# Performance work log

Hardware: AMD Instinct MI355X
Metric: run time of the kernel (lower is better)

The kernel has to match this reference:

```python
import jax, jax.numpy as jnp
import numpy as np

UNITS = 256

def _lstm_step(carry, idx, kernel, rec_kernel, bias, num_chars):
    h, c = carry
    x = jax.nn.one_hot(idx, num_chars, dtype=h.dtype)          # [B, num_chars]
    z = x @ kernel + h @ rec_kernel + bias                      # [B, 4*UNITS]
    i, f, g, o = jnp.split(z, 4, axis=-1)                       # Keras gate order i,f,c,o
    i = jax.nn.sigmoid(i)
    f = jax.nn.sigmoid(f)
    g = jnp.tanh(g)
    o = jax.nn.sigmoid(o)
    c_new = f * c + i * g
    h_new = o * jnp.tanh(c_new)
    return (h_new, c_new), None


def setup_inputs() -> dict:
    key = jax.random.key(0)
    ks = jax.random.split(key, 4)
    num_chars, batch, seq_len = 128, 1024, 512
    x = jax.random.randint(ks[0], (batch, seq_len), 0, num_chars, dtype=jnp.int32)
    kernel = jax.random.normal(ks[1], (num_chars, 4 * UNITS), dtype=jnp.float32) * 0.05
    rec_kernel = jax.random.normal(ks[2], (UNITS, 4 * UNITS), dtype=jnp.float32) * 0.05
    bias = jnp.zeros((4 * UNITS,), dtype=jnp.float32)
    dense_w = jax.random.normal(ks[3], (UNITS, num_chars), dtype=jnp.float32) * 0.05
    dense_b = jnp.zeros((num_chars,), dtype=jnp.float32)
    return {"x": x, "kernel": kernel, "rec_kernel": rec_kernel, "bias": bias,
            "dense_w": dense_w, "dense_b": dense_b}


def reference(x, kernel, rec_kernel, bias, dense_w, dense_b):
    batch = x.shape[0]
    num_chars = kernel.shape[0]
    h0 = jnp.zeros((batch, UNITS), dtype=kernel.dtype)
    c0 = jnp.zeros((batch, UNITS), dtype=kernel.dtype)
    step = lambda carry, idx: _lstm_step(carry, idx, kernel, rec_kernel, bias, num_chars)
    (h, _), _ = jax.lax.scan(step, (h0, c0), x.T)  # scan over time: [S, B]
    logits = h @ dense_w + dense_b                  # [B, num_chars]
    return jax.nn.softmax(logits, axis=-1)
```

## Files before the change

### kernel.cpp

```cpp
#include <hip/hip_runtime.h>
#include <cstdint>

typedef __bf16 bf16x8 __attribute__((ext_vector_type(8)));
typedef float  f32x4  __attribute__((ext_vector_type(4)));

union U4B { uint4 u; bf16x8 b; };
__device__ __forceinline__ bf16x8 as_bf(uint4 u) { U4B x; x.u = u; return x.b; }

__device__ __forceinline__ unsigned short f2b(float x) {
  unsigned int u = __float_as_uint(x);
  unsigned int r = (u + 0x7fffu + ((u >> 16) & 1u)) >> 16;
  return (unsigned short)r;
}
__device__ __forceinline__ float b2f(unsigned int bits_lo16) {
  return __uint_as_float(bits_lo16 << 16);
}

__device__ __forceinline__ float sigm(float x) {
  float e = __builtin_amdgcn_exp2f(x * -1.4426950408889634f);
  return __builtin_amdgcn_rcpf(1.0f + e);
}
__device__ __forceinline__ float tanh_fast(float x) {
  float e = __builtin_amdgcn_exp2f(x * 2.8853900817779268f);
  return 1.0f - 2.0f * __builtin_amdgcn_rcpf(e + 1.0f);
}

__global__ void prep_kernel(const float* __restrict__ rec,
                            const float* __restrict__ kern,
                            const float* __restrict__ bias,
                            const float* __restrict__ dw,
                            unsigned short* __restrict__ recT,
                            unsigned short* __restrict__ kb2,
                            unsigned short* __restrict__ dwT) {
  int id = blockIdx.x * 256 + threadIdx.x;
  if (id < 262144) {
    int colp = id >> 8, k = id & 255;
    int u = colp >> 2, g = colp & 3;
    recT[colp * 256 + k] = f2b(rec[k * 1024 + u + 256 * g]);
  } else if (id < 262144 + 131072) {
    int i = id - 262144;
    int ch = i >> 10, colp = i & 1023;
    int u = colp >> 2, g = colp & 3;
    int oc = u + 256 * g;
    kb2[ch * 1024 + colp] = f2b(kern[ch * 1024 + oc] + bias[oc]);
  } else {
    int i = id - 262144 - 131072;
    int cls = i >> 8, k = i & 255;
    dwT[cls * 256 + k] = f2b(dw[k * 128 + cls]);
  }
}

__global__ __launch_bounds__(512, 2) void lstm_kernel(
    const unsigned short* __restrict__ recT,
    const unsigned short* __restrict__ kb2,
    const unsigned short* __restrict__ dwT,
    const int* __restrict__ x,
    const float* __restrict__ dense_b,
    float* __restrict__ out) {
  __shared__ unsigned short h_buf[2][16][264];
  __shared__ int   x_lds[16][516];
  __shared__ float l_lds[16][132];

  const int tid   = threadIdx.x;
  const int lane  = tid & 63;
  const int wid   = tid >> 6;
  const int row16 = lane & 15;
  const int kg    = lane >> 4;
  const int rbase = blockIdx.x << 4;

  for (int e = tid; e < 16 * 512; e += 512) {
    int r = e >> 9, c = e & 511;
    x_lds[r][c] = x[(rbase + r) * 512 + c];
  }
  for (int e = tid; e < 16 * 264; e += 512) (&h_buf[0][0][0])[e] = 0;

  float c_state[8];
#pragma unroll
  for (int m = 0; m < 8; ++m) c_state[m] = 0.0f;

  const unsigned short* recBase = recT + ((wid * 128 + row16) * 256 + kg * 8);

  __syncthreads();

  for (int t = 0; t < 512; ++t) {
    const int cur = t & 1, nxt = cur ^ 1;

    int idx = x_lds[row16][t];
    const unsigned short* kbBase = kb2 + (idx * 1024 + wid * 128 + kg * 4);
    uint2 kq[8];
#pragma unroll
    for (int m = 0; m < 8; ++m) kq[m] = *(const uint2*)(kbBase + m * 16);

    uint4 hf[8];
#pragma unroll
    for (int k = 0; k < 8; ++k)
      hf[k] = *(const uint4*)&h_buf[cur][row16][k * 32 + kg * 8];

    f32x4 acc[8];
#pragma unroll
    for (int m = 0; m < 8; ++m) {
      uint4 af[8];
#pragma unroll
      for (int k = 0; k < 8; ++k)
        af[k] = *(const uint4*)(recBase + m * 4096 + k * 32);
      f32x4 a = {0.f, 0.f, 0.f, 0.f};
#pragma unroll
      for (int k = 0; k < 8; ++k)
        a = __builtin_amdgcn_mfma_f32_16x16x32_bf16(as_bf(af[k]), as_bf(hf[k]), a, 0, 0, 0);
      acc[m] = a;
    }

#pragma unroll
    for (int m = 0; m < 8; ++m) {
      float zi = acc[m][0] + b2f(kq[m].x & 0xffffu);
      float zf = acc[m][1] + b2f(kq[m].x >> 16);
      float zg = acc[m][2] + b2f(kq[m].y & 0xffffu);
      float zo = acc[m][3] + b2f(kq[m].y >> 16);
      float gi = sigm(zi);
      float gf = sigm(zf);
      float gg = tanh_fast(zg);
      float go = sigm(zo);
      float c  = gf * c_state[m] + gi * gg;
      c_state[m] = c;
      float h  = go * tanh_fast(c);
      h_buf[nxt][row16][(wid * 8 + m) * 4 + kg] = f2b(h);
    }
    __syncthreads();
  }

  {
    const unsigned short* dwBase = dwT + ((wid * 16 + row16) * 256 + kg * 8);
    uint4 hf[8];
#pragma unroll
    for (int k = 0; k < 8; ++k)
      hf[k] = *(const uint4*)&h_buf[0][row16][k * 32 + kg * 8];
    f32x4 la = {0.f, 0.f, 0.f, 0.f};
#pragma unroll
    for (int k = 0; k < 8; ++k) {
      uint4 af = *(const uint4*)(dwBase + k * 32);
      la = __builtin_amdgcn_mfma_f32_16x16x32_bf16(as_bf(af), as_bf(hf[k]), la, 0, 0, 0);
    }
#pragma unroll
    for (int r = 0; r < 4; ++r) {
      int cls = wid * 16 + kg * 4 + r;
      l_lds[row16][cls] = la[r] + dense_b[cls];
    }
  }
  __syncthreads();

  {
    int r = tid >> 5, cg = tid & 31;
    float4 v = *(const float4*)&l_lds[r][cg * 4];
    float mx = fmaxf(fmaxf(v.x, v.y), fmaxf(v.z, v.w));
#pragma unroll
    for (int s = 1; s < 32; s <<= 1) mx = fmaxf(mx, __shfl_xor(mx, s));
    const float L2E = 1.4426950408889634f;
    float e0 = __builtin_amdgcn_exp2f((v.x - mx) * L2E);
    float e1 = __builtin_amdgcn_exp2f((v.y - mx) * L2E);
    float e2 = __builtin_amdgcn_exp2f((v.z - mx) * L2E);
    float e3 = __builtin_amdgcn_exp2f((v.w - mx) * L2E);
    float sm = e0 + e1 + e2 + e3;
#pragma unroll
    for (int s = 1; s < 32; s <<= 1) sm += __shfl_xor(sm, s);
    float inv = __builtin_amdgcn_rcpf(sm);
    float4 o = {e0 * inv, e1 * inv, e2 * inv, e3 * inv};
    *(float4*)&out[(rbase + r) * 128 + cg * 4] = o;
  }
}

extern "C" void kernel_launch(void* const* d_in, const int* in_sizes, int n_in,
                              void* d_out, int out_size, void* d_ws, size_t ws_size,
                              hipStream_t stream) {
  const int*   x      = (const int*)d_in[0];
  const float* kern   = (const float*)d_in[1];
  const float* rec    = (const float*)d_in[2];
  const float* bias   = (const float*)d_in[3];
  const float* dw     = (const float*)d_in[4];
  const float* db     = (const float*)d_in[5];
  float* outp = (float*)d_out;

  unsigned char* ws = (unsigned char*)d_ws;
  unsigned short* recT = (unsigned short*)(ws);
  unsigned short* kb2  = (unsigned short*)(ws + 524288);
  unsigned short* dwT  = (unsigned short*)(ws + 786432);

  prep_kernel<<<1664, 256, 0, stream>>>(rec, kern, bias, dw, recT, kb2, dwT);
  lstm_kernel<<<64, 512, 0, stream>>>(recT, kb2, dwT, x, db, outp);
}
```

Baseline: 3.233 ms.

## Keep recurrent weights resident in registers and LDS, stream the rest

The recurrent weight matrix is now split three ways. Half of each wave's weight tiles are held in VGPRs for the whole sequence and two tiles are staged in LDS. The last two tiles are streamed from global memory with a three-deep software prefetch interleaved with the MFMAs. The MFMA loop is also reordered k-outer so each h fragment is loaded once, and the next token index is prefetched directly from global instead of staging x in LDS. This aims to stop re-reading all recurrent weights from global or L2 every timestep, at the cost of high register pressure (possible spills or lower occupancy under launch_bounds 512,2) and a large LDS footprint.

```diff
diff --git a/kernel.cpp b/kernel.cpp
--- a/kernel.cpp
+++ b/kernel.cpp
@@ -57,9 +57,8 @@
     const int* __restrict__ x,
     const float* __restrict__ dense_b,
     float* __restrict__ out) {
+  __shared__ uint4 A_lds[2][8][512];
   __shared__ unsigned short h_buf[2][16][264];
-  __shared__ int   x_lds[16][516];
-  __shared__ float l_lds[16][132];
 
   const int tid   = threadIdx.x;
   const int lane  = tid & 63;
@@ -68,48 +67,88 @@
   const int kg    = lane >> 4;
   const int rbase = blockIdx.x << 4;
 
-  for (int e = tid; e < 16 * 512; e += 512) {
-    int r = e >> 9, c = e & 511;
-    x_lds[r][c] = x[(rbase + r) * 512 + c];
-  }
+  const unsigned short* recBase = recT + ((wid * 128 + row16) * 256 + kg * 8);
+
+  uint4 af[4][8];
+#pragma unroll
+  for (int m = 0; m < 4; ++m)
+#pragma unroll
+    for (int k = 0; k < 8; ++k) {
+      af[m][k] = *(const uint4*)(recBase + m * 4096 + k * 32);
+      asm volatile("" : "+v"(af[m][k].x), "+v"(af[m][k].y),
+                        "+v"(af[m][k].z), "+v"(af[m][k].w));
+    }
+
+#pragma unroll
+  for (int s = 0; s < 2; ++s)
+#pragma unroll
+    for (int k = 0; k < 8; ++k)
+      A_lds[s][k][wid * 64 + lane] = *(const uint4*)(recBase + (4 + s) * 4096 + k * 32);
+
+  const unsigned short* sb6 = recBase + 6 * 4096;
+  const unsigned short* sb7 = recBase + 7 * 4096;
+  uint4 st6[8], st7[8];
+#pragma unroll
+  for (int k = 0; k < 3; ++k) {
+    st6[k] = *(const uint4*)(sb6 + k * 32);
+    st7[k] = *(const uint4*)(sb7 + k * 32);
+  }
+
   for (int e = tid; e < 16 * 264; e += 512) (&h_buf[0][0][0])[e] = 0;
 
   float c_state[8];
 #pragma unroll
   for (int m = 0; m < 8; ++m) c_state[m] = 0.0f;
 
-  const unsigned short* recBase = recT + ((wid * 128 + row16) * 256 + kg * 8);
+  const int* xrow = x + (rbase + row16) * 512;
+  int idx_cur = xrow[0];
 
   __syncthreads();
 
+  int cur = 0;
+  const unsigned aoff_base = (wid * 64 + lane) * 16;
+
+#pragma unroll 1
   for (int t = 0; t < 512; ++t) {
-    const int cur = t & 1, nxt = cur ^ 1;
-
-    int idx = x_lds[row16][t];
-    const unsigned short* kbBase = kb2 + (idx * 1024 + wid * 128 + kg * 4);
+    unsigned z6 = 0, zL = 0;
+    asm volatile("" : "+v"(z6), "+v"(zL));
+    const unsigned short* sb6v = sb6 + z6;
+    const unsigned short* sb7v = sb7 + z6;
+    const unsigned aoff = aoff_base + zL;
+
+    int idx_next = xrow[(t + 1 < 512) ? t + 1 : 511];
+
+    const unsigned short* hrow = &h_buf[cur][row16][0];
+    const unsigned short* kb = kb2 + (idx_cur * 1024 + wid * 128 + kg * 4);
     uint2 kq[8];
-#pragma unroll
-    for (int m = 0; m < 8; ++m) kq[m] = *(const uint2*)(kbBase + m * 16);
-
-    uint4 hf[8];
-#pragma unroll
-    for (int k = 0; k < 8; ++k)
-      hf[k] = *(const uint4*)&h_buf[cur][row16][k * 32 + kg * 8];
 
     f32x4 acc[8];
 #pragma unroll
-    for (int m = 0; m < 8; ++m) {
-      uint4 af[8];
-#pragma unroll
-      for (int k = 0; k < 8; ++k)
-        af[k] = *(const uint4*)(recBase + m * 4096 + k * 32);
-      f32x4 a = {0.f, 0.f, 0.f, 0.f};
-#pragma unroll
-      for (int k = 0; k < 8; ++k)
-        a = __builtin_amdgcn_mfma_f32_16x16x32_bf16(as_bf(af[k]), as_bf(hf[k]), a, 0, 0, 0);
-      acc[m] = a;
-    }
-
+    for (int m = 0; m < 8; ++m) acc[m] = f32x4{0.f, 0.f, 0.f, 0.f};
+
+#pragma unroll
+    for (int k = 0; k < 8; ++k) {
+      uint4 hf = *(const uint4*)(hrow + k * 32 + kg * 8);
+      acc[0] = __builtin_amdgcn_mfma_f32_16x16x32_bf16(as_bf(af[0][k]), as_bf(hf), acc[0], 0, 0, 0);
+      acc[1] = __builtin_amdgcn_mfma_f32_16x16x32_bf16(as_bf(af[1][k]), as_bf(hf), acc[1], 0, 0, 0);
+      acc[2] = __builtin_amdgcn_mfma_f32_16x16x32_bf16(as_bf(af[2][k]), as_bf(hf), acc[2], 0, 0, 0);
+      acc[3] = __builtin_amdgcn_mfma_f32_16x16x32_bf16(as_bf(af[3][k]), as_bf(hf), acc[3], 0, 0, 0);
+      uint4 a4 = *(const uint4*)((const char*)A_lds + (0 * 8 + k) * 8192 + aoff);
+      acc[4] = __builtin_amdgcn_mfma_f32_16x16x32_bf16(as_bf(a4), as_bf(hf), acc[4], 0, 0, 0);
+      uint4 a5 = *(const uint4*)((const char*)A_lds + (1 * 8 + k) * 8192 + aoff);
+      acc[5] = __builtin_amdgcn_mfma_f32_16x16x32_bf16(as_bf(a5), as_bf(hf), acc[5], 0, 0, 0);
+      acc[6] = __builtin_amdgcn_mfma_f32_16x16x32_bf16(as_bf(st6[k]), as_bf(hf), acc[6], 0, 0, 0);
+      acc[7] = __builtin_amdgcn_mfma_f32_16x16x32_bf16(as_bf(st7[k]), as_bf(hf), acc[7], 0, 0, 0);
+      const int kp = (k + 3) & 7;
+      st6[kp] = *(const uint4*)(sb6v + kp * 32);
+      st7[kp] = *(const uint4*)(sb7v + kp * 32);
+      if (k == 4) {
+#pragma unroll
+        for (int m = 0; m < 8; ++m) kq[m] = *(const uint2*)(kb + m * 16);
+      }
+    }
+
+    unsigned short* hn = &h_buf[cur ^ 1][row16][wid * 32 + kg];
 #pragma unroll
     for (int m = 0; m < 8; ++m) {
       float zi = acc[m][0] + b2f(kq[m].x & 0xffffu);
@@ -123,11 +162,14 @@
       float c  = gf * c_state[m] + gi * gg;
       c_state[m] = c;
       float h  = go * tanh_fast(c);
-      h_buf[nxt][row16][(wid * 8 + m) * 4 + kg] = f2b(h);
+      hn[m * 4] = f2b(h);
     }
     __syncthreads();
-  }
-
+    cur ^= 1;
+    idx_cur = idx_next;
+  }
+
+  float (*l_lds)[132] = (float (*)[132])A_lds;
   {
     const unsigned short* dwBase = dwT + ((wid * 16 + row16) * 256 + kg * 8);
     uint4 hf[8];
@@ -137,8 +179,8 @@
     f32x4 la = {0.f, 0.f, 0.f, 0.f};
 #pragma unroll
     for (int k = 0; k < 8; ++k) {
-      uint4 af = *(const uint4*)(dwBase + k * 32);
-      la = __builtin_amdgcn_mfma_f32_16x16x32_bf16(as_bf(af), as_bf(hf[k]), la, 0, 0, 0);
+      uint4 afd = *(const uint4*)(dwBase + k * 32);
+      la = __builtin_amdgcn_mfma_f32_16x16x32_bf16(as_bf(afd), as_bf(hf[k]), la, 0, 0, 0);
     }
 #pragma unroll
     for (int r = 0; r < 4; ++r) {
```

New measurement: 2.824 ms. -12.6%, faster.

## Keep recurrent weights resident in AGPRs and vectorize swizzled h-state writes

Applied to the files above, without the earlier changes.

The bf16 recurrent weight fragments are loaded once before the time loop and pinned in accumulator registers, so the 512 steps no longer re-read them from global/L2. The hidden-unit K ordering is permuted in the prep kernel so each lane writes its eight h values as one 16-byte LDS store, and the h buffer uses an XOR swizzle to cut bank conflicts. The x tile is no longer staged in LDS; the next index is prefetched from global one step ahead. This costs a very large register footprint pinned to two waves per EU, and depends on the compiler keeping the 256 AGPR values without spilling.

```diff
diff --git a/kernel.cpp b/kernel.cpp
--- a/kernel.cpp
+++ b/kernel.cpp
@@ -23,6 +23,10 @@
 __device__ __forceinline__ float tanh_fast(float x) {
   float e = __builtin_amdgcn_exp2f(x * 2.8853900817779268f);
   return 1.0f - 2.0f * __builtin_amdgcn_rcpf(e + 1.0f);
+}
+
+__device__ __forceinline__ int kperm_u(int k) {
+  return ((k >> 3) & 7) * 32 + (k & 7) * 4 + (k >> 6);
 }
 
 __global__ void prep_kernel(const float* __restrict__ rec,
@@ -35,30 +39,32 @@
   int id = blockIdx.x * 256 + threadIdx.x;
   if (id < 262144) {
     int colp = id >> 8, k = id & 255;
-    int u = colp >> 2, g = colp & 3;
-    recT[colp * 256 + k] = f2b(rec[k * 1024 + u + 256 * g]);
+    int u = kperm_u(k);
+    int oc = (colp >> 2) + 256 * (colp & 3);
+    recT[colp * 256 + k] = f2b(rec[u * 1024 + oc]);
   } else if (id < 262144 + 131072) {
     int i = id - 262144;
     int ch = i >> 10, colp = i & 1023;
-    int u = colp >> 2, g = colp & 3;
-    int oc = u + 256 * g;
+    int oc = (colp >> 2) + 256 * (colp & 3);
     kb2[ch * 1024 + colp] = f2b(kern[ch * 1024 + oc] + bias[oc]);
   } else {
     int i = id - 262144 - 131072;
     int cls = i >> 8, k = i & 255;
-    dwT[cls * 256 + k] = f2b(dw[k * 128 + cls]);
-  }
-}
-
-__global__ __launch_bounds__(512, 2) void lstm_kernel(
+    int u = kperm_u(k);
+    dwT[cls * 256 + k] = f2b(dw[u * 128 + cls]);
+  }
+}
+
+__global__ __launch_bounds__(512)
+__attribute__((amdgpu_waves_per_eu(2, 2)))
+void lstm_kernel(
     const unsigned short* __restrict__ recT,
     const unsigned short* __restrict__ kb2,
     const unsigned short* __restrict__ dwT,
     const int* __restrict__ x,
     const float* __restrict__ dense_b,
     float* __restrict__ out) {
-  __shared__ unsigned short h_buf[2][16][264];
-  __shared__ int   x_lds[16][516];
+  __shared__ unsigned short h_buf[2][16][288];
   __shared__ float l_lds[16][132];
 
   const int tid   = threadIdx.x;
@@ -68,77 +74,93 @@
   const int kg    = lane >> 4;
   const int rbase = blockIdx.x << 4;
 
-  for (int e = tid; e < 16 * 512; e += 512) {
-    int r = e >> 9, c = e & 511;
-    x_lds[r][c] = x[(rbase + r) * 512 + c];
-  }
-  for (int e = tid; e < 16 * 264; e += 512) (&h_buf[0][0][0])[e] = 0;
+  const unsigned short* recBase = recT + ((wid * 128 + row16) * 256 + kg * 8);
+  uint4 af[8][8];
+#pragma unroll
+  for (int m = 0; m < 8; ++m)
+#pragma unroll
+    for (int k = 0; k < 8; ++k) {
+      af[m][k] = *(const uint4*)(recBase + m * 4096 + k * 32);
+      asm volatile("" : "+a"(af[m][k].x), "+a"(af[m][k].y),
+                        "+a"(af[m][k].z), "+a"(af[m][k].w));
+    }
+
+  for (int e = tid; e < 2 * 16 * 288 / 8; e += 512)
+    ((uint4*)h_buf)[e] = uint4{0, 0, 0, 0};
 
   float c_state[8];
 #pragma unroll
   for (int m = 0; m < 8; ++m) c_state[m] = 0.0f;
 
-  const unsigned short* recBase = recT + ((wid * 128 + row16) * 256 + kg * 8);
+  const int* xrow = x + (rbase + row16) * 512;
+  int idx = xrow[0];
+
+  char* lds = (char*)&h_buf[0][0][0];
+  const unsigned swz  = (unsigned)((row16 & 7) << 4);
+  const unsigned rowB = (unsigned)(row16 * 576);
+  const unsigned kgo  = (unsigned)(kg * 16);
+  const unsigned wrOff = rowB + (((unsigned)(kg * 128 + wid * 16)) ^ swz);
 
   __syncthreads();
 
+  int cur = 0;
+#pragma unroll 1
   for (int t = 0; t < 512; ++t) {
-    const int cur = t & 1, nxt = cur ^ 1;
-
-    int idx = x_lds[row16][t];
-    const unsigned short* kbBase = kb2 + (idx * 1024 + wid * 128 + kg * 4);
+    const unsigned short* kb = kb2 + (idx * 1024 + wid * 128 + kg * 4);
     uint2 kq[8];
 #pragma unroll
-    for (int m = 0; m < 8; ++m) kq[m] = *(const uint2*)(kbBase + m * 16);
-
-    uint4 hf[8];
-#pragma unroll
-    for (int k = 0; k < 8; ++k)
-      hf[k] = *(const uint4*)&h_buf[cur][row16][k * 32 + kg * 8];
-
+    for (int m = 0; m < 8; ++m) kq[m] = *(const uint2*)(kb + m * 16);
+    int idx_next = xrow[(t + 1 < 512) ? t + 1 : 511];
+
+    const char* hrdRow = lds + cur * 9216 + rowB;
     f32x4 acc[8];
 #pragma unroll
-    for (int m = 0; m < 8; ++m) {
-      uint4 af[8];
-#pragma unroll
-      for (int k = 0; k < 8; ++k)
-        af[k] = *(const uint4*)(recBase + m * 4096 + k * 32);
-      f32x4 a = {0.f, 0.f, 0.f, 0.f};
-#pragma unroll
-      for (int k = 0; k < 8; ++k)
-        a = __builtin_amdgcn_mfma_f32_16x16x32_bf16(as_bf(af[k]), as_bf(hf[k]), a, 0, 0, 0);
-      acc[m] = a;
-    }
-
-#pragma unroll
-    for (int m = 0; m < 8; ++m) {
-      float zi = acc[m][0] + b2f(kq[m].x & 0xffffu);
-      float zf = acc[m][1] + b2f(kq[m].x >> 16);
-      float zg = acc[m][2] + b2f(kq[m].y & 0xffffu);
-      float zo = acc[m][3] + b2f(kq[m].y >> 16);
-      float gi = sigm(zi);
-      float gf = sigm(zf);
-      float gg = tanh_fast(zg);
-      float go = sigm(zo);
-      float c  = gf * c_state[m] + gi * gg;
-      c_state[m] = c;
-      float h  = go * tanh_fast(c);
-      h_buf[nxt][row16][(wid * 8 + m) * 4 + kg] = f2b(h);
-    }
+    for (int m = 0; m < 8; ++m) acc[m] = f32x4{0.f, 0.f, 0.f, 0.f};
+#pragma unroll
+    for (int k = 0; k < 8; ++k) {
+      uint4 hf = *(const uint4*)(hrdRow + ((((unsigned)(k * 64)) + kgo) ^ swz));
+      acc[0] = __builtin_amdgcn_mfma_f32_16x16x32_bf16(as_bf(af[0][k]), as_bf(hf), acc[0], 0, 0, 0);
+      acc[1] = __builtin_amdgcn_mfma_f32_16x16x32_bf16(as_bf(af[1][k]), as_bf(hf), acc[1], 0, 0, 0);
+      acc[2] = __builtin_amdgcn_mfma_f32_16x16x32_bf16(as_bf(af[2][k]), as_bf(hf), acc[2], 0, 0, 0);
+      acc[3] = __builtin_amdgcn_mfma_f32_16x16x32_bf16(as_bf(af[3][k]), as_bf(hf), acc[3], 0, 0, 0);
+      acc[4] = __builtin_amdgcn_mfma_f32_16x16x32_bf16(as_bf(af[4][k]), as_bf(hf), acc[4], 0, 0, 0);
+      acc[5] = __builtin_amdgcn_mfma_f32_16x16x32_bf16(as_bf(af[5][k]), as_bf(hf), acc[5], 0, 0, 0);
+      acc[6] = __builtin_amdgcn_mfma_f32_16x16x32_bf16(as_bf(af[6][k]), as_bf(hf), acc[6], 0, 0, 0);
+      acc[7] = __builtin_amdgcn_mfma_f32_16x16x32_bf16(as_bf(af[7][k]), as_bf(hf), acc[7], 0, 0, 0);
+    }
+
+    unsigned hw[4];
+#pragma unroll
+    for (int p = 0; p < 4; ++p) {
+      unsigned short hb[2];
+#pragma unroll
+      for (int q = 0; q < 2; ++q) {
+        const int m = p * 2 + q;
+        float zi = acc[m][0] + b2f(kq[m].x & 0xffffu);
+        float zf = acc[m][1] + b2f(kq[m].x >> 16);
+        float zg = acc[m][2] + b2f(kq[m].y & 0xffffu);
+        float zo = acc[m][3] + b2f(kq[m].y >> 16);
+        float c  = sigm(zf) * c_state[m] + sigm(zi) * tanh_fast(zg);
+        c_state[m] = c;
+        hb[q] = f2b(sigm(zo) * tanh_fast(c));
+      }
+      hw[p] = (unsigned)hb[0] | ((unsigned)hb[1] << 16);
+    }
+    *(uint4*)(lds + (cur ^ 1) * 9216 + wrOff) = uint4{hw[0], hw[1], hw[2], hw[3]};
+
     __syncthreads();
+    cur ^= 1;
+    idx = idx_next;
   }
 
   {
     const unsigned short* dwBase = dwT + ((wid * 16 + row16) * 256 + kg * 8);
-    uint4 hf[8];
-#pragma unroll
-    for (int k = 0; k < 8; ++k)
-      hf[k] = *(const uint4*)&h_buf[0][row16][k * 32 + kg * 8];
     f32x4 la = {0.f, 0.f, 0.f, 0.f};
 #pragma unroll
     for (int k = 0; k < 8; ++k) {
-      uint4 af = *(const uint4*)(dwBase + k * 32);
-      la = __builtin_amdgcn_mfma_f32_16x16x32_bf16(as_bf(af), as_bf(hf[k]), la, 0, 0, 0);
+      uint4 hf  = *(const uint4*)(lds + rowB + ((((unsigned)(k * 64)) + kgo) ^ swz));
+      uint4 afd = *(const uint4*)(dwBase + k * 32);
+      la = __builtin_amdgcn_mfma_f32_16x16x32_bf16(as_bf(afd), as_bf(hf), la, 0, 0, 0);
     }
 #pragma unroll
     for (int r = 0; r < 4; ++r) {
@@ -153,7 +175,7 @@
     float4 v = *(const float4*)&l_lds[r][cg * 4];
     float mx = fmaxf(fmaxf(v.x, v.y), fmaxf(v.z, v.w));
 #pragma unroll
-    for (int s = 1; s < 32; s <<= 1) mx = fmaxf(mx, __shfl_xor(mx, s));
+    for (int sh = 1; sh < 32; sh <<= 1) mx = fmaxf(mx, __shfl_xor(mx, sh));
     const float L2E = 1.4426950408889634f;
     float e0 = __builtin_amdgcn_exp2f((v.x - mx) * L2E);
     float e1 = __builtin_amdgcn_exp2f((v.y - mx) * L2E);
@@ -161,7 +183,7 @@
     float e3 = __builtin_amdgcn_exp2f((v.w - mx) * L2E);
     float sm = e0 + e1 + e2 + e3;
 #pragma unroll
-    for (int s = 1; s < 32; s <<= 1) sm += __shfl_xor(sm, s);
+    for (int sh = 1; sh < 32; sh <<= 1) sm += __shfl_xor(sm, sh);
     float inv = __builtin_amdgcn_rcpf(sm);
     float4 o = {e0 * inv, e1 * inv, e2 * inv, e3 * inv};
     *(float4*)&out[(rbase + r) * 128 + cg * 4] = o;
```

Result: slower. 4.203 ms (+30.0%).
